# Kernel tuning notes

Measured on AMD Instinct MI355X. Metric: run time of the kernel, lower is better.

Reference implementation:

```python
import math
import jax, jax.numpy as jnp
import numpy as np

WIN = 8
NUM_HEADS = 8

def _rel_pos_index(win):
    coords = np.stack(np.meshgrid(np.arange(win), np.arange(win), indexing='ij'))
    cf = coords.reshape(2, -1)
    rel = cf[:, :, None] - cf[:, None, :]
    rel = rel.transpose(1, 2, 0).copy()
    rel[:, :, 0] += win - 1
    rel[:, :, 1] += win - 1
    rel[:, :, 0] *= 2 * win - 1
    return rel.sum(-1)  # [N, N]

def _shift_mask(H, W, win, Ho, Wo):
    m = np.zeros((H, W))
    h_slices = (slice(0, -win), slice(-win, -Ho), slice(-Ho, None)) if Ho > 0 else (slice(0, None),)
    w_slices = (slice(0, -win), slice(-win, -Wo), slice(-Wo, None)) if Wo > 0 else (slice(0, None),)
    cnt = 0
    for hs in h_slices:
        for ws in w_slices:
            m[hs, ws] = cnt
            cnt += 1
    mw = m.reshape(H // win, win, W // win, win).transpose(0, 2, 1, 3).reshape(-1, win * win)
    d = mw[:, None, :] - mw[:, :, None]
    return np.where(d != 0, -100.0, 0.0).astype(np.float32)  # [nW, N, N]

def _ln(x, g, b, eps=1e-5):
    mu = jnp.mean(x, axis=-1, keepdims=True)
    var = jnp.mean((x - mu) ** 2, axis=-1, keepdims=True)
    return (x - mu) / jnp.sqrt(var + eps) * g + b

def _win_part(x, win):
    B, H, W, C = x.shape
    x = x.reshape(B, H // win, win, W // win, win, C).transpose(0, 1, 3, 2, 4, 5)
    return x.reshape(-1, win * win, C)

def _win_rev(w, win, H, W):
    C = w.shape[-1]
    B = w.shape[0] // ((H // win) * (W // win))
    x = w.reshape(B, H // win, W // win, win, win, C).transpose(0, 1, 3, 2, 4, 5)
    return x.reshape(B, H, W, C)

def setup_inputs() -> dict:
    key = jax.random.key(0)
    ks = jax.random.split(key, 10)
    B, L, C, hid = 4, 32768, 256, 1024
    s = 0.02
    return {
        'x': jax.random.normal(ks[0], (B, L, C), jnp.float32),
        'norm1_g': jnp.ones((C,), jnp.float32),
        'norm1_b': jnp.zeros((C,), jnp.float32),
        'wq': jax.random.normal(ks[1], (C, C), jnp.float32) * s,
        'bq': jnp.zeros((C,), jnp.float32),
        'wv': jax.random.normal(ks[2], (C, C), jnp.float32) * s,
        'bv': jnp.zeros((C,), jnp.float32),
        'rpb': jax.random.normal(ks[3], (225, NUM_HEADS), jnp.float32) * s,
        'wproj': jax.random.normal(ks[4], (C, C), jnp.float32) * s,
        'bproj': jnp.zeros((C,), jnp.float32),
        'norm2_g': jnp.ones((C,), jnp.float32),
        'norm2_b': jnp.zeros((C,), jnp.float32),
        'w1': jax.random.normal(ks[5], (C, hid), jnp.float32) * s,
        'b1': jnp.zeros((hid,), jnp.float32),
        'dw_k': jax.random.normal(ks[6], (hid, 1, 3, 3), jnp.float32) * s,
        'dw_b': jnp.zeros((hid,), jnp.float32),
        'w2': jax.random.normal(ks[7], (hid, C), jnp.float32) * s,
        'b2': jnp.zeros((C,), jnp.float32),
        'H_offset': 3,
        'W_offset': 5,
    }

def reference(x, norm1_g, norm1_b, wq, bq, wv, bv, rpb, wproj, bproj,
              norm2_g, norm2_b, w1, b1, dw_k, dw_b, w2, b2, H_offset, W_offset):
    B, L, C = x.shape
    H = int(round(math.sqrt(L * 2)))
    W = int(round(math.sqrt(L // 2)))
    win, h = WIN, NUM_HEADS
    hd = C // h
    N = win * win
    nW = (H // win) * (W // win)
    scale = hd ** -0.5

    shortcut = x
    xn = _ln(x, norm1_g, norm1_b)
    q = xn @ wq + bq
    v = xn @ wv + bv
    q = q.reshape(B, H, W, C)
    v = v.reshape(B, H, W, C)
    k = q  # module uses k = q (shared)

    q = jnp.roll(q, (-H_offset, -W_offset), axis=(1, 2))
    k = jnp.roll(k, (-H_offset, -W_offset), axis=(1, 2))
    v = jnp.roll(v, (-H_offset, -W_offset), axis=(1, 2))

    qw = _win_part(q, win).reshape(-1, N, h, hd).transpose(0, 2, 1, 3)
    kw = _win_part(k, win).reshape(-1, N, h, hd).transpose(0, 2, 1, 3)
    vw = _win_part(v, win).reshape(-1, N, h, hd).transpose(0, 2, 1, 3)

    attn = jnp.einsum('bhnd,bhmd->bhnm', qw * scale, kw)
    bias = rpb[jnp.asarray(_rel_pos_index(win).reshape(-1))].reshape(N, N, h).transpose(2, 0, 1)
    attn = attn + bias[None]
    mask = jnp.asarray(_shift_mask(H, W, win, int(H_offset), int(W_offset)))
    attn = (attn.reshape(B, nW, h, N, N) + mask[None, :, None]).reshape(-1, h, N, N)
    attn = jax.nn.softmax(attn, axis=-1)

    y = jnp.einsum('bhnm,bhmd->bhnd', attn, vw).transpose(0, 2, 1, 3).reshape(-1, N, C)
    y = y @ wproj + bproj
    y = _win_rev(y.reshape(-1, win, win, C), win, H, W)
    y = jnp.roll(y, (H_offset, W_offset), axis=(1, 2)).reshape(B, L, C)

    x = shortcut + y

    # LeFF
    xn2 = _ln(x, norm2_g, norm2_b)
    t = jax.nn.gelu(xn2 @ w1 + b1, approximate=False)  # [B, L, hid]
    t = t.reshape(B, H, W, -1).transpose(0, 3, 1, 2)   # NCHW
    t = jax.lax.conv_general_dilated(t, dw_k, (1, 1), 'SAME',
                                     feature_group_count=t.shape[1],
                                     dimension_numbers=('NCHW', 'OIHW', 'NCHW'))
    t = jax.nn.gelu(t + dw_b[None, :, None, None], approximate=False)
    t = t.transpose(0, 2, 3, 1).reshape(B, L, -1)
    t = t @ w2 + b2
    return x + t
```

## Files before the change

### kernel.cpp

```cpp
#include <hip/hip_runtime.h>
#include <stdint.h>
#include <math.h>

#define H_IMG 256
#define W_IMG 128
#define LTOK  32768
#define BATCH 4
#define CDIM  256
#define HIDDIM 1024
#define NHEAD 8
#define HD    32
#define MROWS 131072

typedef __attribute__((ext_vector_type(8))) short short8;
typedef __attribute__((ext_vector_type(4))) float f32x4;

__device__ __forceinline__ float bf2f(unsigned u) {
  union { unsigned u; float f; } c; c.u = u << 16; return c.f;
}
__device__ __forceinline__ unsigned short f2bf(float f) {
  union { float f; unsigned u; } c; c.f = f;
  unsigned r = c.u + 0x7fffu + ((c.u >> 16) & 1u);
  return (unsigned short)(r >> 16);
}
__device__ __forceinline__ void unpack8(uint4 t, float* dst) {
  dst[0] = bf2f(t.x & 0xffffu); dst[1] = bf2f(t.x >> 16);
  dst[2] = bf2f(t.y & 0xffffu); dst[3] = bf2f(t.y >> 16);
  dst[4] = bf2f(t.z & 0xffffu); dst[5] = bf2f(t.z >> 16);
  dst[6] = bf2f(t.w & 0xffffu); dst[7] = bf2f(t.w >> 16);
}
__device__ __forceinline__ float gelu_f(float x) {
  return 0.5f * x * (1.0f + erff(x * 0.70710678118654752f));
}
__device__ __forceinline__ void gload_lds16(const void* g, void* l) {
  __builtin_amdgcn_global_load_lds(
      (const __attribute__((address_space(1))) unsigned int*)g,
      (__attribute__((address_space(3))) unsigned int*)l, 16, 0, 0);
}

__global__ __launch_bounds__(256) void wconv_kernel(
    const float* __restrict__ w, unsigned short* __restrict__ wt, int K, int N) {
  __shared__ float t[32][33];
  const int k0 = blockIdx.x * 32, n0 = blockIdx.y * 32;
  const int tx = threadIdx.x & 31, ty = threadIdx.x >> 5;
#pragma unroll
  for (int i = 0; i < 4; ++i)
    t[ty + 8 * i][tx] = w[(size_t)(k0 + ty + 8 * i) * N + n0 + tx];
  __syncthreads();
#pragma unroll
  for (int i = 0; i < 4; ++i)
    wt[(size_t)(n0 + ty + 8 * i) * K + k0 + tx] = f2bf(t[tx][ty + 8 * i]);
}

__global__ __launch_bounds__(256) void ln_kernel(
    const float* __restrict__ x, const float* __restrict__ g,
    const float* __restrict__ b, unsigned short* __restrict__ out) {
  const int wave = threadIdx.x >> 6;
  const int lane = threadIdx.x & 63;
  const size_t row = (size_t)blockIdx.x * 4 + wave;
  float4 f = ((const float4*)(x + row * CDIM))[lane];
  float s  = f.x + f.y + f.z + f.w;
  float sq = f.x*f.x + f.y*f.y + f.z*f.z + f.w*f.w;
#pragma unroll
  for (int o = 32; o > 0; o >>= 1) { s += __shfl_down(s, o); sq += __shfl_down(sq, o); }
  s = __shfl(s, 0); sq = __shfl(sq, 0);
  const float mu = s * (1.0f / CDIM);
  const float var = sq * (1.0f / CDIM) - mu * mu;
  const float rstd = rsqrtf(var + 1e-5f);
  float4 gg = ((const float4*)g)[lane];
  float4 bb = ((const float4*)b)[lane];
  unsigned short o4[4];
  o4[0] = f2bf((f.x - mu) * rstd * gg.x + bb.x);
  o4[1] = f2bf((f.y - mu) * rstd * gg.y + bb.y);
  o4[2] = f2bf((f.z - mu) * rstd * gg.z + bb.z);
  o4[3] = f2bf((f.w - mu) * rstd * gg.w + bb.w);
  *(uint2*)(out + row * CDIM + lane * 4) = *(uint2*)o4;
}

template<int EPI, int PERM>
__global__ __launch_bounds__(256) void mgemm(
    const unsigned short* __restrict__ A, const unsigned short* __restrict__ Bt,
    const float* __restrict__ bias, const float* __restrict__ bias2,
    const float* __restrict__ res, void* __restrict__ outp, void* __restrict__ outp2,
    int K, int ldc, const int* __restrict__ pHo, const int* __restrict__ pWo) {
  __shared__ unsigned short As[2][128][32];
  __shared__ unsigned short Bs[2][128][32];
  const int tid = threadIdx.x;
  const int w = tid >> 6, lane = tid & 63;
  const int m0 = blockIdx.x * 128, n0 = blockIdx.y * 128;
  const int wm = (w & 1) * 64, wn = (w >> 1) * 64;
  const int srow = lane >> 2;
  const int csrc = (lane & 3) ^ (srow & 3);
  f32x4 acc[4][4];
#pragma unroll
  for (int mi = 0; mi < 4; ++mi)
#pragma unroll
    for (int ni = 0; ni < 4; ++ni)
#pragma unroll
      for (int r = 0; r < 4; ++r) acc[mi][ni][r] = 0.0f;

  const int kg = lane >> 4, ml = lane & 15;
  const int nt = K >> 5;

  auto STAGE = [&](int kk, int buf) {
#pragma unroll
    for (int i = 0; i < 2; ++i) {
      const int rl = w * 32 + i * 16 + srow;
      gload_lds16(A + (size_t)(m0 + rl) * K + kk + csrc * 8, &As[buf][w * 32 + i * 16][0]);
      gload_lds16(Bt + (size_t)(n0 + rl) * K + kk + csrc * 8, &Bs[buf][w * 32 + i * 16][0]);
    }
  };

  STAGE(0, 0);
  for (int t = 0; t < nt; ++t) {
    const int cur = t & 1;
    if (t + 1 < nt) {
      STAGE((t + 1) << 5, cur ^ 1);
      asm volatile("s_waitcnt vmcnt(4)" ::: "memory");
    } else {
      asm volatile("s_waitcnt vmcnt(0)" ::: "memory");
    }
    __builtin_amdgcn_s_barrier();
    __builtin_amdgcn_sched_barrier(0);
    short8 af[4], bg[4];
#pragma unroll
    for (int mi = 0; mi < 4; ++mi) {
      const int r = wm + mi * 16 + ml;
      af[mi] = *(const short8*)&As[cur][r][(kg ^ (r & 3)) * 8];
    }
#pragma unroll
    for (int ni = 0; ni < 4; ++ni) {
      const int r = wn + ni * 16 + ml;
      bg[ni] = *(const short8*)&Bs[cur][r][(kg ^ (r & 3)) * 8];
    }
#pragma unroll
    for (int mi = 0; mi < 4; ++mi)
#pragma unroll
      for (int ni = 0; ni < 4; ++ni)
        acc[mi][ni] = __builtin_amdgcn_mfma_f32_16x16x32_bf16(af[mi], bg[ni], acc[mi][ni], 0, 0, 0);
    __builtin_amdgcn_sched_barrier(0);
    __builtin_amdgcn_s_barrier();
  }

  if constexpr (PERM == 4) {
    const int Ho = pHo[0], Wo = pWo[0];
    const bool vhalf = (n0 >= 256);
    size_t rbase[4][4];
#pragma unroll
    for (int mi = 0; mi < 4; ++mi) {
#pragma unroll
      for (int r = 0; r < 4; ++r) {
        const int m = m0 + wm + mi * 16 + kg * 4 + r;
        const int bimg = m >> 15, l = m & 32767;
        int hr = (l >> 7) - Ho; if (hr < 0) hr += H_IMG;
        int wr = (l & 127) - Wo; if (wr < 0) wr += W_IMG;
        const int win = (hr >> 3) * 16 + (wr >> 3);
        const int t64 = (hr & 7) * 8 + (wr & 7);
        rbase[mi][r] = (size_t)(bimg * 512 + win) * 16384 + (vhalf ? t64 : t64 * 32);
      }
    }
    unsigned short* dst = (unsigned short*)(vhalf ? outp2 : outp);
    const float* bp = vhalf ? bias2 : bias;
#pragma unroll
    for (int ni = 0; ni < 4; ++ni) {
      const int nn = n0 + wn + ni * 16 + ml - (vhalf ? 256 : 0);
      const float bn = bp[nn];
      const size_t noff = (size_t)(nn >> 5) * 2048 + (vhalf ? (nn & 31) * 64 : (nn & 31));
#pragma unroll
      for (int mi = 0; mi < 4; ++mi)
#pragma unroll
        for (int r = 0; r < 4; ++r)
          dst[rbase[mi][r] + noff] = f2bf(acc[mi][ni][r] + bn);
    }
  } else {
#pragma unroll
    for (int ni = 0; ni < 4; ++ni) {
      const int n = n0 + wn + ni * 16 + ml;
      const float bn = bias[n];
#pragma unroll
      for (int mi = 0; mi < 4; ++mi) {
#pragma unroll
        for (int r = 0; r < 4; ++r) {
          const int m = m0 + wm + mi * 16 + kg * 4 + r;
          const size_t idx = (size_t)m * ldc + n;
          float val = acc[mi][ni][r] + bn;
          if (EPI == 1) {
            ((float*)outp)[idx] = val + res[idx];
          } else if (EPI == 2) {
            ((unsigned short*)outp)[idx] = f2bf(gelu_f(val));
          } else {
            ((unsigned short*)outp)[idx] = f2bf(val);
          }
        }
      }
    }
  }
}

__global__ __launch_bounds__(256, 3) void attn_kernel(
    const unsigned short* __restrict__ q, const unsigned short* __restrict__ v,
    const float* __restrict__ rpb, const int* __restrict__ pHo,
    const int* __restrict__ pWo, unsigned short* __restrict__ yout) {
  __shared__ unsigned short Pb[4][4096];
  __shared__ float bias_w[4][228];
  __shared__ int reg_s[64];
  const int tid = threadIdx.x;
  const int w = tid >> 6, lane = tid & 63;
  const int g = lane >> 4, c = lane & 15;
  const int wb = blockIdx.x;
  const int b = wb >> 9, wloc = wb & 511;
  const int wh = wloc >> 4, ww = wloc & 15;
  const int Ho = pHo[0], Wo = pWo[0];
  const bool edge = (wh == (H_IMG / 8 - 1)) || (ww == (W_IMG / 8 - 1));
  if (w == 0) {
    const int dy = lane >> 3, dx = lane & 7;
    const int hr = wh * 8 + dy, wr = ww * 8 + dx;
    const int rh = (hr < H_IMG - 8) ? 0 : ((hr < H_IMG - Ho) ? 1 : 2);
    const int rw = (wr < W_IMG - 8) ? 0 : ((wr < W_IMG - Wo) ? 1 : 2);
    reg_s[lane] = rh * 3 + rw;
  }
  __syncthreads();

  const float scale = 0.17677669529663687f;
  const int dxk = c & 7, dyk0 = c >> 3;
  const int base_l = 112 - dyk0 * 15 - dxk;
  const size_t hbase0 = (size_t)(b * 512 + wloc) * 8;
  const int dy2 = lane >> 3, dx2 = lane & 7;
  int h2 = wh * 8 + dy2 + Ho; if (h2 >= H_IMG) h2 -= H_IMG;
  int w2_ = ww * 8 + dx2 + Wo; if (w2_ >= W_IMG) w2_ -= W_IMG;
  const size_t otok = (size_t)b * LTOK + (size_t)h2 * W_IMG + w2_;

  for (int p2 = 0; p2 < 2; ++p2) {
    const int hh = w + 4 * p2;
    const unsigned short* qh = q + (hbase0 + hh) * 2048;
    const unsigned short* vh = v + (hbase0 + hh) * 2048;
#pragma unroll
    for (int i = 0; i < 4; ++i) {
      const int idx = lane + 64 * i;
      if (idx < 225) bias_w[w][idx] = rpb[idx * 8 + hh];
    }
    short8 q4[4];
#pragma unroll
    for (int mi = 0; mi < 4; ++mi)
      q4[mi] = *(const short8*)(qh + (16 * mi + c) * 32 + g * 8);
    short8 vf[2][2];
#pragma unroll
    for (int s2 = 0; s2 < 2; ++s2)
#pragma unroll
      for (int n2 = 0; n2 < 2; ++n2)
        vf[s2][n2] = *(const short8*)(vh + (16 * n2 + c) * 64 + 32 * s2 + 8 * g);
    f32x4 acc[4][4];
#pragma unroll
    for (int mi = 0; mi < 4; ++mi)
#pragma unroll
      for (int nj = 0; nj < 4; ++nj)
#pragma unroll
        for (int r = 0; r < 4; ++r) acc[mi][nj][r] = 0.0f;
#pragma unroll
    for (int mi = 0; mi < 4; ++mi)
#pragma unroll
      for (int nj = 0; nj < 4; ++nj)
        acc[mi][nj] = __builtin_amdgcn_mfma_f32_16x16x32_bf16(q4[mi], q4[nj], acc[mi][nj], 0, 0, 0);
    int regk[4];
    if (edge) {
#pragma unroll
      for (int nj = 0; nj < 4; ++nj) regk[nj] = reg_s[16 * nj + c];
    }
    unsigned short* Pp = &Pb[w][0];
    float ivr[4][4];
#pragma unroll
    for (int mi = 0; mi < 4; ++mi) {
#pragma unroll
      for (int r = 0; r < 4; ++r) {
        const int qq = 16 * mi + 4 * g + r;
        const int rb = (qq >> 3) * 15 + (qq & 7) + base_l;
        float sv[4];
#pragma unroll
        for (int nj = 0; nj < 4; ++nj)
          sv[nj] = acc[mi][nj][r] * scale + bias_w[w][rb - 30 * nj];
        if (edge) {
          const int regq = reg_s[qq];
#pragma unroll
          for (int nj = 0; nj < 4; ++nj)
            if (regq != regk[nj]) sv[nj] -= 100.0f;
        }
        float e0 = __expf(sv[0]), e1 = __expf(sv[1]);
        float e2 = __expf(sv[2]), e3 = __expf(sv[3]);
        float sm = e0 + e1 + e2 + e3;
        sm += __shfl_xor(sm, 1);
        sm += __shfl_xor(sm, 2);
        sm += __shfl_xor(sm, 4);
        sm += __shfl_xor(sm, 8);
        ivr[mi][r] = __builtin_amdgcn_rcpf(sm);
        const int rowoff = qq * 64, sw = qq & 7;
        Pp[rowoff + ((dyk0 ^ sw) * 8)       + dxk] = f2bf(e0);
        Pp[rowoff + (((2 + dyk0) ^ sw) * 8) + dxk] = f2bf(e1);
        Pp[rowoff + (((4 + dyk0) ^ sw) * 8) + dxk] = f2bf(e2);
        Pp[rowoff + (((6 + dyk0) ^ sw) * 8) + dxk] = f2bf(e3);
      }
    }
    f32x4 oacc[4][2];
#pragma unroll
    for (int mi = 0; mi < 4; ++mi)
#pragma unroll
      for (int n2 = 0; n2 < 2; ++n2)
#pragma unroll
        for (int r = 0; r < 4; ++r) oacc[mi][n2][r] = 0.0f;
#pragma unroll
    for (int s2 = 0; s2 < 2; ++s2) {
      short8 pa[4];
#pragma unroll
      for (int mi = 0; mi < 4; ++mi) {
        const int qq2 = 16 * mi + c;
        pa[mi] = *(const short8*)&Pp[qq2 * 64 + (((4 * s2 + g) ^ (qq2 & 7)) * 8)];
      }
#pragma unroll
      for (int mi = 0; mi < 4; ++mi)
#pragma unroll
        for (int n2 = 0; n2 < 2; ++n2)
          oacc[mi][n2] = __builtin_amdgcn_mfma_f32_16x16x32_bf16(pa[mi], vf[s2][n2], oacc[mi][n2], 0, 0, 0);
    }
    unsigned short* Ost = Pp;
#pragma unroll
    for (int mi = 0; mi < 4; ++mi)
#pragma unroll
      for (int n2 = 0; n2 < 2; ++n2)
#pragma unroll
        for (int r = 0; r < 4; ++r)
          Ost[(16 * mi + 4 * g + r) * 40 + 16 * n2 + c] = f2bf(oacc[mi][n2][r] * ivr[mi][r]);
    uint4* op = (uint4*)(yout + otok * CDIM + hh * 32);
#pragma unroll
    for (int u = 0; u < 4; ++u)
      op[u] = *(const uint4*)&Ost[lane * 40 + u * 8];
  }
}

__global__ __launch_bounds__(256) void dwconv_kernel(
    const unsigned short* __restrict__ t1b, const float* __restrict__ k9,
    const float* __restrict__ bias, unsigned short* __restrict__ t2b,
    int hr0, int band_rows) {
  const int c = blockIdx.y * 256 + (threadIdx.x & 31) * 8;
  const int tok = blockIdx.x * 8 + (threadIdx.x >> 5);
  const int h = hr0 + (tok >> 7), wcol = tok & 127;
  float wreg[8][9];
#pragma unroll
  for (int j = 0; j < 8; ++j)
#pragma unroll
    for (int tp = 0; tp < 9; ++tp) wreg[j][tp] = k9[(c + j) * 9 + tp];
  float bb[8];
#pragma unroll
  for (int j = 0; j < 8; ++j) bb[j] = bias[c + j];
  float a[8] = {};
#pragma unroll
  for (int ky = 0; ky < 3; ++ky) {
    const int hy = h + ky - 1;
    if ((unsigned)hy >= (unsigned)H_IMG) continue;
    const int brow = (tok >> 7) + ky;
#pragma unroll
    for (int kx = 0; kx < 3; ++kx) {
      const int wx = wcol + kx - 1;
      if ((unsigned)wx >= (unsigned)W_IMG) continue;
      const uint4 tv = *(const uint4*)(
          t1b + ((size_t)(brow * 128 + wx)) * HIDDIM + c);
      float f8[8];
      unpack8(tv, f8);
      const int tp = ky * 3 + kx;
#pragma unroll
      for (int j = 0; j < 8; ++j) a[j] += f8[j] * wreg[j][tp];
    }
  }
  unsigned short o[8];
#pragma unroll
  for (int j = 0; j < 8; ++j) o[j] = f2bf(gelu_f(a[j] + bb[j]));
  *(uint4*)(t2b + (size_t)tok * HIDDIM + c) = *(uint4*)o;
}

extern "C" void kernel_launch(void* const* d_in, const int* in_sizes, int n_in,
                              void* d_out, int out_size, void* d_ws, size_t ws_size,
                              hipStream_t stream) {
  (void)in_sizes; (void)n_in; (void)out_size; (void)ws_size;
  const float* x     = (const float*)d_in[0];
  const float* n1g   = (const float*)d_in[1];
  const float* n1b   = (const float*)d_in[2];
  const float* wq    = (const float*)d_in[3];
  const float* bq    = (const float*)d_in[4];
  const float* wv    = (const float*)d_in[5];
  const float* bv    = (const float*)d_in[6];
  const float* rpb   = (const float*)d_in[7];
  const float* wproj = (const float*)d_in[8];
  const float* bproj = (const float*)d_in[9];
  const float* n2g   = (const float*)d_in[10];
  const float* n2b   = (const float*)d_in[11];
  const float* w1    = (const float*)d_in[12];
  const float* b1    = (const float*)d_in[13];
  const float* dwk   = (const float*)d_in[14];
  const float* dwb   = (const float*)d_in[15];
  const float* w2    = (const float*)d_in[16];
  const float* b2    = (const float*)d_in[17];
  const int*   pHo   = (const int*)d_in[18];
  const int*   pWo   = (const int*)d_in[19];
  float* out = (float*)d_out;

  char* wsb = (char*)d_ws;
  unsigned short* r0     = (unsigned short*)wsb;
  unsigned short* wqt    = (unsigned short*)(wsb + 67108864ull);
  unsigned short* wvt    = (unsigned short*)(wsb + 67108864ull + 131072ull);
  unsigned short* wprojt = (unsigned short*)(wsb + 67108864ull + 262144ull);
  unsigned short* w1t    = (unsigned short*)(wsb + 67108864ull + 393216ull);
  unsigned short* w2t    = (unsigned short*)(wsb + 67108864ull + 917504ull);
  unsigned short* t1b    = (unsigned short*)(wsb + 68550656ull);
  unsigned short* t2b    = (unsigned short*)(wsb + 68550656ull + 25690112ull);
  unsigned short* vb     = (unsigned short*)d_out;
  unsigned short* qb     = (unsigned short*)((char*)d_out + 67108864ull);

  wconv_kernel<<<dim3(8, 8),  256, 0, stream>>>(wq,    wqt,    CDIM, CDIM);
  wconv_kernel<<<dim3(8, 8),  256, 0, stream>>>(wv,    wvt,    CDIM, CDIM);
  wconv_kernel<<<dim3(8, 8),  256, 0, stream>>>(wproj, wprojt, CDIM, CDIM);
  wconv_kernel<<<dim3(8, 32), 256, 0, stream>>>(w1,    w1t,    CDIM, HIDDIM);
  wconv_kernel<<<dim3(32, 8), 256, 0, stream>>>(w2,    w2t,    HIDDIM, CDIM);

  ln_kernel<<<32768, 256, 0, stream>>>(x, n1g, n1b, r0);
  mgemm<0, 4><<<dim3(1024, 4), 256, 0, stream>>>(
      r0, wqt, bq, bv, nullptr, qb, vb, CDIM, CDIM, pHo, pWo);
  attn_kernel<<<dim3(2048), 256, 0, stream>>>(qb, vb, rpb, pHo, pWo, r0);
  mgemm<1, 0><<<dim3(1024, 2), 256, 0, stream>>>(
      r0, wprojt, bproj, nullptr, x, out, nullptr, CDIM, CDIM, pHo, pWo);
  ln_kernel<<<32768, 256, 0, stream>>>(out, n2g, n2b, r0);
  for (int bi = 0; bi < BATCH; ++bi) {
    for (int hr0 = 0; hr0 < H_IMG; ) {
      const int br = (H_IMG - hr0 >= 96) ? 96 : (H_IMG - hr0);
      const int r_start = (hr0 > 0) ? hr0 - 1 : 0;
      const int r_end = (hr0 + br <= H_IMG - 1) ? hr0 + br : H_IMG - 1;
      const int nrows = r_end - r_start + 1;
      const unsigned short* Aff1 = r0 + ((size_t)bi * LTOK + (size_t)r_start * W_IMG) * CDIM;
      unsigned short* t1dst = t1b + (size_t)(r_start - hr0 + 1) * W_IMG * HIDDIM;
      mgemm<2, 0><<<dim3(nrows, 8), 256, 0, stream>>>(
          Aff1, w1t, b1, nullptr, nullptr, t1dst, nullptr, CDIM, HIDDIM, pHo, pWo);
      dwconv_kernel<<<dim3(br * 16, 4), 256, 0, stream>>>(t1b, dwk, dwb, t2b, hr0, br);
      const size_t btok = (size_t)bi * LTOK + (size_t)hr0 * W_IMG;
      mgemm<1, 0><<<dim3(br, 2), 256, 0, stream>>>(
          t2b, w2t, b2, nullptr, out + btok * CDIM, out + btok * CDIM, nullptr,
          HIDDIM, CDIM, pHo, pWo);
      hr0 += br;
    }
  }
}
```

Measured before the change: 1.644 ms.

## Triple-buffer GEMM staging and store Q/V interleaved with in-LDS V transpose

The GEMM main loop goes from double to triple buffering in LDS, prefetching two K-tiles ahead with adjusted vmcnt waits so more global loads are in flight. The QV projection epilogue now writes Q and V into one interleaved per-window buffer with token-major layout for both, replacing the previous scattered transposed V stores. The attention kernel reads V contiguously and transposes it through LDS before building MFMA fragments. This trades coalesced global stores for extra LDS traffic and more LDS per GEMM block, which may lower occupancy.

New measurement: 1.595 ms. -3.0%, faster.

```diff
diff --git a/kernel.cpp b/kernel.cpp
--- a/kernel.cpp
+++ b/kernel.cpp
@@ -81,10 +81,10 @@
 __global__ __launch_bounds__(256) void mgemm(
     const unsigned short* __restrict__ A, const unsigned short* __restrict__ Bt,
     const float* __restrict__ bias, const float* __restrict__ bias2,
-    const float* __restrict__ res, void* __restrict__ outp, void* __restrict__ outp2,
+    const float* __restrict__ res, void* __restrict__ outp,
     int K, int ldc, const int* __restrict__ pHo, const int* __restrict__ pWo) {
-  __shared__ unsigned short As[2][128][32];
-  __shared__ unsigned short Bs[2][128][32];
+  __shared__ unsigned short As[3][128][32];
+  __shared__ unsigned short Bs[3][128][32];
   const int tid = threadIdx.x;
   const int w = tid >> 6, lane = tid & 63;
   const int m0 = blockIdx.x * 128, n0 = blockIdx.y * 128;
@@ -112,10 +112,13 @@
   };
 
   STAGE(0, 0);
+  if (nt > 1) STAGE(32, 1);
   for (int t = 0; t < nt; ++t) {
-    const int cur = t & 1;
-    if (t + 1 < nt) {
-      STAGE((t + 1) << 5, cur ^ 1);
+    const int cur = t % 3;
+    if (t + 2 < nt) {
+      STAGE((t + 2) << 5, (t + 2) % 3);
+      asm volatile("s_waitcnt vmcnt(8)" ::: "memory");
+    } else if (t + 1 < nt) {
       asm volatile("s_waitcnt vmcnt(4)" ::: "memory");
     } else {
       asm volatile("s_waitcnt vmcnt(0)" ::: "memory");
@@ -144,7 +147,6 @@
 
   if constexpr (PERM == 4) {
     const int Ho = pHo[0], Wo = pWo[0];
-    const bool vhalf = (n0 >= 256);
     size_t rbase[4][4];
 #pragma unroll
     for (int mi = 0; mi < 4; ++mi) {
@@ -156,16 +158,15 @@
         int wr = (l & 127) - Wo; if (wr < 0) wr += W_IMG;
         const int win = (hr >> 3) * 16 + (wr >> 3);
         const int t64 = (hr & 7) * 8 + (wr & 7);
-        rbase[mi][r] = (size_t)(bimg * 512 + win) * 16384 + (vhalf ? t64 : t64 * 32);
+        rbase[mi][r] = (size_t)(bimg * 512 + win) * 32768 + t64 * 32;
       }
     }
-    unsigned short* dst = (unsigned short*)(vhalf ? outp2 : outp);
-    const float* bp = vhalf ? bias2 : bias;
+    unsigned short* dst = (unsigned short*)outp;
 #pragma unroll
     for (int ni = 0; ni < 4; ++ni) {
-      const int nn = n0 + wn + ni * 16 + ml - (vhalf ? 256 : 0);
-      const float bn = bp[nn];
-      const size_t noff = (size_t)(nn >> 5) * 2048 + (vhalf ? (nn & 31) * 64 : (nn & 31));
+      const int nn = n0 + wn + ni * 16 + ml;
+      const float bn = (nn < 256) ? bias[nn] : bias2[nn - 256];
+      const size_t noff = (size_t)(nn >> 5) * 2048 + (nn & 31);
 #pragma unroll
       for (int mi = 0; mi < 4; ++mi)
 #pragma unroll
@@ -198,9 +199,9 @@
 }
 
 __global__ __launch_bounds__(256, 3) void attn_kernel(
-    const unsigned short* __restrict__ q, const unsigned short* __restrict__ v,
-    const float* __restrict__ rpb, const int* __restrict__ pHo,
-    const int* __restrict__ pWo, unsigned short* __restrict__ yout) {
+    const unsigned short* __restrict__ qv, const float* __restrict__ rpb,
+    const int* __restrict__ pHo, const int* __restrict__ pWo,
+    unsigned short* __restrict__ yout) {
   __shared__ unsigned short Pb[4][4096];
   __shared__ float bias_w[4][228];
   __shared__ int reg_s[64];
@@ -224,7 +225,7 @@
   const float scale = 0.17677669529663687f;
   const int dxk = c & 7, dyk0 = c >> 3;
   const int base_l = 112 - dyk0 * 15 - dxk;
-  const size_t hbase0 = (size_t)(b * 512 + wloc) * 8;
+  const size_t hbase = (size_t)(b * 512 + wloc) * 32768;
   const int dy2 = lane >> 3, dx2 = lane & 7;
   int h2 = wh * 8 + dy2 + Ho; if (h2 >= H_IMG) h2 -= H_IMG;
   int w2_ = ww * 8 + dx2 + Wo; if (w2_ >= W_IMG) w2_ -= W_IMG;
@@ -232,8 +233,10 @@
 
   for (int p2 = 0; p2 < 2; ++p2) {
     const int hh = w + 4 * p2;
-    const unsigned short* qh = q + (hbase0 + hh) * 2048;
-    const unsigned short* vh = v + (hbase0 + hh) * 2048;
+    const unsigned short* qh = qv + hbase + hh * 2048;
+    const unsigned short* vh = qv + hbase + (8 + hh) * 2048;
+    const uint4* vp = (const uint4*)(vh + lane * 32);
+    uint4 a0 = vp[0], a1 = vp[1], a2 = vp[2], a3 = vp[3];
 #pragma unroll
     for (int i = 0; i < 4; ++i) {
       const int idx = lane + 64 * i;
@@ -243,12 +246,6 @@
 #pragma unroll
     for (int mi = 0; mi < 4; ++mi)
       q4[mi] = *(const short8*)(qh + (16 * mi + c) * 32 + g * 8);
-    short8 vf[2][2];
-#pragma unroll
-    for (int s2 = 0; s2 < 2; ++s2)
-#pragma unroll
-      for (int n2 = 0; n2 < 2; ++n2)
-        vf[s2][n2] = *(const short8*)(vh + (16 * n2 + c) * 64 + 32 * s2 + 8 * g);
     f32x4 acc[4][4];
 #pragma unroll
     for (int mi = 0; mi < 4; ++mi)
@@ -261,6 +258,22 @@
 #pragma unroll
       for (int nj = 0; nj < 4; ++nj)
         acc[mi][nj] = __builtin_amdgcn_mfma_f32_16x16x32_bf16(q4[mi], q4[nj], acc[mi][nj], 0, 0, 0);
+    unsigned short* vt = &Pb[w][0];
+    {
+      unsigned tmp[16] = {a0.x,a0.y,a0.z,a0.w,a1.x,a1.y,a1.z,a1.w,
+                          a2.x,a2.y,a2.z,a2.w,a3.x,a3.y,a3.z,a3.w};
+#pragma unroll
+      for (int d2 = 0; d2 < 16; ++d2) {
+        vt[(2 * d2) * 72 + lane]     = (unsigned short)(tmp[d2] & 0xffffu);
+        vt[(2 * d2 + 1) * 72 + lane] = (unsigned short)(tmp[d2] >> 16);
+      }
+    }
+    short8 vf[2][2];
+#pragma unroll
+    for (int s2 = 0; s2 < 2; ++s2)
+#pragma unroll
+      for (int n2 = 0; n2 < 2; ++n2)
+        vf[s2][n2] = *(const short8*)&vt[(16 * n2 + c) * 72 + 32 * s2 + 8 * g];
     int regk[4];
     if (edge) {
 #pragma unroll
@@ -410,8 +423,7 @@
   unsigned short* w2t    = (unsigned short*)(wsb + 67108864ull + 917504ull);
   unsigned short* t1b    = (unsigned short*)(wsb + 68550656ull);
   unsigned short* t2b    = (unsigned short*)(wsb + 68550656ull + 25690112ull);
-  unsigned short* vb     = (unsigned short*)d_out;
-  unsigned short* qb     = (unsigned short*)((char*)d_out + 67108864ull);
+  unsigned short* qvb    = (unsigned short*)d_out;
 
   wconv_kernel<<<dim3(8, 8),  256, 0, stream>>>(wq,    wqt,    CDIM, CDIM);
   wconv_kernel<<<dim3(8, 8),  256, 0, stream>>>(wv,    wvt,    CDIM, CDIM);
@@ -421,10 +433,10 @@
 
   ln_kernel<<<32768, 256, 0, stream>>>(x, n1g, n1b, r0);
   mgemm<0, 4><<<dim3(1024, 4), 256, 0, stream>>>(
-      r0, wqt, bq, bv, nullptr, qb, vb, CDIM, CDIM, pHo, pWo);
-  attn_kernel<<<dim3(2048), 256, 0, stream>>>(qb, vb, rpb, pHo, pWo, r0);
+      r0, wqt, bq, bv, nullptr, qvb, CDIM, CDIM, pHo, pWo);
+  attn_kernel<<<dim3(2048), 256, 0, stream>>>(qvb, rpb, pHo, pWo, r0);
   mgemm<1, 0><<<dim3(1024, 2), 256, 0, stream>>>(
-      r0, wprojt, bproj, nullptr, x, out, nullptr, CDIM, CDIM, pHo, pWo);
+      r0, wprojt, bproj, nullptr, x, out, CDIM, CDIM, pHo, pWo);
   ln_kernel<<<32768, 256, 0, stream>>>(out, n2g, n2b, r0);
   for (int bi = 0; bi < BATCH; ++bi) {
     for (int hr0 = 0; hr0 < H_IMG; ) {
@@ -435,11 +447,11 @@
       const unsigned short* Aff1 = r0 + ((size_t)bi * LTOK + (size_t)r_start * W_IMG) * CDIM;
       unsigned short* t1dst = t1b + (size_t)(r_start - hr0 + 1) * W_IMG * HIDDIM;
       mgemm<2, 0><<<dim3(nrows, 8), 256, 0, stream>>>(
-          Aff1, w1t, b1, nullptr, nullptr, t1dst, nullptr, CDIM, HIDDIM, pHo, pWo);
+          Aff1, w1t, b1, nullptr, nullptr, t1dst, CDIM, HIDDIM, pHo, pWo);
       dwconv_kernel<<<dim3(br * 16, 4), 256, 0, stream>>>(t1b, dwk, dwb, t2b, hr0, br);
       const size_t btok = (size_t)bi * LTOK + (size_t)hr0 * W_IMG;
       mgemm<1, 0><<<dim3(br, 2), 256, 0, stream>>>(
-          t2b, w2t, b2, nullptr, out + btok * CDIM, out + btok * CDIM, nullptr,
+          t2b, w2t, b2, nullptr, out + btok * CDIM, out + btok * CDIM,
           HIDDIM, CDIM, pHo, pWo);
       hr0 += br;
     }
```
